# Kernel optimization log

Measured on AMD Instinct MI355X. Metric: run time of the kernel, lower is better.

## Reference

```python
import jax, jax.numpy as jnp
import numpy as np

N_HEAD = 8
D_HEAD = 32  # d_model=256 // n_head=8
SCALE = 1.0 / (D_HEAD ** 0.5)
CLIP = 10.0


def _rel_shift(x):
    # x: [qlen, klen, B, nh]; Transformer-XL relative shift along axis 1
    qlen, klen = x.shape[0], x.shape[1]
    zero_pad = jnp.zeros((qlen, 1) + x.shape[2:], dtype=x.dtype)
    x_pad = jnp.concatenate([zero_pad, x], axis=1)          # [qlen, klen+1, B, nh]
    x_pad = x_pad.reshape((klen + 1, qlen) + x.shape[2:])   # row-major reshape (torch .view)
    return x_pad[1:].reshape(x.shape)


def setup_inputs() -> dict:
    key = jax.random.key(0)
    ks = jax.random.split(key, 7)
    S, B, H = 1024, 8, 256
    return {
        "q": jax.random.normal(ks[0], (S, B, H), dtype=jnp.float32),
        "k": jax.random.normal(ks[1], (S, B, H), dtype=jnp.float32),
        "v": jax.random.normal(ks[2], (S, B, H), dtype=jnp.float32),
        "r": jax.random.normal(ks[3], (S, 1, H), dtype=jnp.float32),
        "bias_u": jax.random.normal(ks[4], (N_HEAD, D_HEAD), dtype=jnp.float32),
        "bias_v": jax.random.normal(ks[5], (N_HEAD, D_HEAD), dtype=jnp.float32),
        "mask": jax.random.randint(ks[6], (S, S, B), 0, 2).astype(jnp.bool_),
    }


def reference(q, k, v, r, bias_u, bias_v, mask):
    qlen, bsz = q.shape[0], q.shape[1]
    klen, rlen = k.shape[0], r.shape[0]
    q = q.reshape(qlen, bsz, N_HEAD, D_HEAD)
    k = k.reshape(klen, bsz, N_HEAD, D_HEAD)
    v = v.reshape(klen, bsz, N_HEAD, D_HEAD)
    r = r.reshape(rlen, N_HEAD, D_HEAD)

    AC = jnp.einsum('ibnd,jbnd->ijbn', q + bias_u, k)   # content term
    BD = jnp.einsum('ibnd,jnd->ijbn', q + bias_v, r)    # position term
    BD = _rel_shift(BD)

    score = (AC + BD) * SCALE
    score = CLIP * jnp.tanh(score)                      # clip > 0 path

    weight = jax.nn.softmax(score, axis=1)              # softmax over klen

    # mask is not None path: masked softmax of head-mean logits
    logits = score.mean(axis=-1)                        # [qlen, klen, B]
    logits = jnp.where(mask, -jnp.inf, logits)
    probs = jax.nn.softmax(logits, axis=1)

    out = jnp.einsum('ijbn,jbnd->ibnd', weight, v)
    out = out.reshape(qlen, bsz, N_HEAD * D_HEAD)
    return out, probs
```

## Files before the change

### kernel.cpp

```cpp
#include <hip/hip_runtime.h>
#include <hip/hip_fp16.h>

#define S 1024
#define B 8
#define NH 8
#define DH 32
#define HID 256
#define SCALEF 0.17677669529663687f

typedef __attribute__((ext_vector_type(8))) _Float16 f16x8;
typedef __attribute__((ext_vector_type(4))) _Float16 f16x4;
typedef __attribute__((ext_vector_type(4))) float f32x4;
#define MFMAH(a, b, c) __builtin_amdgcn_mfma_f32_16x16x32_f16(a, b, c, 0, 0, 0)

#define OFF_K_H 0
#define OFF_K_L 2560
#define OFF_VT  5120
#define OFF_RL  7680
#define OFF_RH  12800
#define OFF_P   17920
#define LDS_HF  20480

__device__ __forceinline__ void splitf16_4(const float4 x, _Float16* dh, _Float16* dl) {
  f16x4 h, l;
  h.x = (_Float16)x.x; h.y = (_Float16)x.y; h.z = (_Float16)x.z; h.w = (_Float16)x.w;
  l.x = (_Float16)(x.x - (float)h.x); l.y = (_Float16)(x.y - (float)h.y);
  l.z = (_Float16)(x.z - (float)h.z); l.w = (_Float16)(x.w - (float)h.w);
  *(f16x4*)dh = h; *(f16x4*)dl = l;
}
__device__ __forceinline__ void cvtf16_4(const float4 x, _Float16* d) {
  f16x4 h;
  h.x = (_Float16)x.x; h.y = (_Float16)x.y; h.z = (_Float16)x.z; h.w = (_Float16)x.w;
  *(f16x4*)d = h;
}

__global__ __launch_bounds__(256)
void relattn_mfma_86028194939537(const float* __restrict__ q, const float* __restrict__ k,
                                 const float* __restrict__ v, const float* __restrict__ r,
                                 const float* __restrict__ bu, const float* __restrict__ bv,
                                 float* __restrict__ out, __half* __restrict__ sws) {
  __shared__ _Float16 sm[LDS_HF];
  const int t = threadIdx.x;
  const int lane = t & 63, w = t >> 6;
  const int quad = lane >> 4, jn = lane & 15;
  const int bid = blockIdx.x;
  const int b = bid & 7, it = (bid >> 3) & 15, n = bid >> 7;
  const int i0 = it << 6, iw0 = i0 + (w << 4);
  const int colq = quad << 3;
  const int i16 = i0 >> 4;

  f16x8 qu_h, qu_l, qv_h, qv_l, qn_h, qn_l;
  {
    const float* bup = bu + n * DH + colq;
    const float* bvp = bv + n * DH + colq;
    const float* qp = q + (size_t)(iw0 + jn) * 2048 + b * HID + n * DH + colq;
    int r1 = iw0 + 1 + jn; if (r1 > S - 1) r1 = S - 1;
    const float* qp1 = q + (size_t)r1 * 2048 + b * HID + n * DH + colq;
#pragma unroll
    for (int e = 0; e < 8; ++e) {
      float xu = qp[e] + bup[e], xv = qp[e] + bvp[e], xn = qp1[e] + bvp[e];
      _Float16 h;
      h = (_Float16)xu; qu_h[e] = h; qu_l[e] = (_Float16)(xu - (float)h);
      h = (_Float16)xv; qv_h[e] = h; qv_l[e] = (_Float16)(xv - (float)h);
      h = (_Float16)xn; qn_h[e] = h; qn_l[e] = (_Float16)(xn - (float)h);
    }
  }

  __half* swsr[4];
#pragma unroll
  for (int g = 0; g < 4; ++g) {
    const int qr = (quad << 2) + g;
    swsr[g] = sws + (((size_t)(iw0 + qr) * 8 + b) * 8 + n) * 1024 + jn;
  }

  f32x4 out0 = {0.f, 0.f, 0.f, 0.f}, out1 = {0.f, 0.f, 0.f, 0.f};
  float ls[4] = {0.f, 0.f, 0.f, 0.f};

  {
    int j = t >> 3, d4 = (t & 7) << 2;
    const size_t g = (size_t)j * 2048 + b * HID + n * DH + d4;
    float4 kx = *(const float4*)(k + g);
    float4 vx = *(const float4*)(v + g);
    splitf16_4(kx, &sm[OFF_K_H + j * 40 + d4], &sm[OFF_K_L + j * 40 + d4]);
    sm[OFF_VT + (d4 + 0) * 40 + j] = (_Float16)vx.x;
    sm[OFF_VT + (d4 + 1) * 40 + j] = (_Float16)vx.y;
    sm[OFF_VT + (d4 + 2) * 40 + j] = (_Float16)vx.z;
    sm[OFF_VT + (d4 + 3) * 40 + j] = (_Float16)vx.w;
  }
#pragma unroll
  for (int p = 0; p < 3; ++p) {
    int ti = 2 * p + (t >> 7), row = (t >> 3) & 15, d4 = (t & 7) << 2;
    {
      int kL = 60 - i16 + ti;
      int tg = (kL << 4) + row; tg = tg < 0 ? 0 : (tg > S - 1 ? S - 1 : tg);
      float4 rv = *(const float4*)(r + (size_t)tg * HID + n * DH + d4);
      int sl = (kL + 72) & 7;
      cvtf16_4(rv, &sm[OFF_RL + (sl * 16 + row) * 40 + d4]);
    }
    {
      int kH = -i16 - 3 + ti;
      int tg = (kH << 4) - 17 + row; tg = tg < 0 ? 0 : (tg > S - 1 ? S - 1 : tg);
      float4 rv = *(const float4*)(r + (size_t)tg * HID + n * DH + d4);
      int sl = (kH + 72) & 7;
      cvtf16_4(rv, &sm[OFF_RH + (sl * 16 + row) * 40 + d4]);
    }
  }

  for (int jt = 0; jt < 32; ++jt) {
    const int j0 = jt << 5;
    __syncthreads();

    if (jt < 31) {
      int j = t >> 3, d4 = (t & 7) << 2;
      const int nbuf = ((jt + 1) & 1) * 1280;
      const size_t g = (size_t)(j0 + 32 + j) * 2048 + b * HID + n * DH + d4;
      float4 kx = *(const float4*)(k + g);
      float4 vx = *(const float4*)(v + g);
      splitf16_4(kx, &sm[OFF_K_H + nbuf + j * 40 + d4], &sm[OFF_K_L + nbuf + j * 40 + d4]);
      sm[OFF_VT + nbuf + (d4 + 0) * 40 + j] = (_Float16)vx.x;
      sm[OFF_VT + nbuf + (d4 + 1) * 40 + j] = (_Float16)vx.y;
      sm[OFF_VT + nbuf + (d4 + 2) * 40 + j] = (_Float16)vx.z;
      sm[OFF_VT + nbuf + (d4 + 3) * 40 + j] = (_Float16)vx.w;
    }
    {
      int ti = t >> 7, row = (t >> 3) & 15, d4 = (t & 7) << 2;
      {
        int kL = 66 + 2 * jt - i16 + ti;
        int tg = (kL << 4) + row; tg = tg < 0 ? 0 : (tg > S - 1 ? S - 1 : tg);
        float4 rv = *(const float4*)(r + (size_t)tg * HID + n * DH + d4);
        int sl = (kL + 72) & 7;
        cvtf16_4(rv, &sm[OFF_RL + (sl * 16 + row) * 40 + d4]);
      }
      {
        int kH = 2 * jt - i16 + 3 + ti;
        int tg = (kH << 4) - 17 + row; tg = tg < 0 ? 0 : (tg > S - 1 ? S - 1 : tg);
        float4 rv = *(const float4*)(r + (size_t)tg * HID + n * DH + d4);
        int sl = (kH + 72) & 7;
        cvtf16_4(rv, &sm[OFF_RH + (sl * 16 + row) * 40 + d4]);
      }
    }

    const int buf = (jt & 1) * 1280;
    const bool lowA = (j0 <= iw0 + 15);
    const bool highA = (j0 + 29 >= iw0);

    f32x4 ac0 = {0.f, 0.f, 0.f, 0.f}, ac1 = {0.f, 0.f, 0.f, 0.f};
    {
      f16x8 b0h = *(const f16x8*)&sm[OFF_K_H + buf + jn * 40 + colq];
      f16x8 b0l = *(const f16x8*)&sm[OFF_K_L + buf + jn * 40 + colq];
      f16x8 b1h = *(const f16x8*)&sm[OFF_K_H + buf + (16 + jn) * 40 + colq];
      f16x8 b1l = *(const f16x8*)&sm[OFF_K_L + buf + (16 + jn) * 40 + colq];
      ac0 = MFMAH(qu_h, b0h, ac0); ac0 = MFMAH(qu_h, b0l, ac0); ac0 = MFMAH(qu_l, b0h, ac0);
      ac1 = MFMAH(qu_h, b1h, ac1); ac1 = MFMAH(qu_h, b1l, ac1); ac1 = MFMAH(qu_l, b1h, ac1);
    }

    f32x4 zl0 = {0.f,0.f,0.f,0.f}, zl1 = {0.f,0.f,0.f,0.f}, zl2 = {0.f,0.f,0.f,0.f};
    f32x4 zh0 = {0.f,0.f,0.f,0.f}, zh1 = {0.f,0.f,0.f,0.f}, zh2 = {0.f,0.f,0.f,0.f};
    if (lowA) {
#pragma unroll
      for (int z = 0; z < 3; ++z) {
        int kL = 63 - i16 - w + 2 * jt + z;
        int sl = (kL + 72) & 7;
        f16x8 rr = *(const f16x8*)&sm[OFF_RL + (sl * 16 + jn) * 40 + colq];
        f32x4 acc = {0.f, 0.f, 0.f, 0.f};
        acc = MFMAH(qv_h, rr, acc); acc = MFMAH(qv_l, rr, acc);
        if (z == 0) zl0 = acc; else if (z == 1) zl1 = acc; else zl2 = acc;
      }
    }
    if (highA) {
#pragma unroll
      for (int z = 0; z < 3; ++z) {
        int kH = 2 * jt - i16 - w + z;
        int sl = (kH + 72) & 7;
        f16x8 rr = *(const f16x8*)&sm[OFF_RH + (sl * 16 + jn) * 40 + colq];
        f32x4 acc = {0.f, 0.f, 0.f, 0.f};
        acc = MFMAH(qn_h, rr, acc); acc = MFMAH(qn_l, rr, acc);
        if (z == 0) zh0 = acc; else if (z == 1) zh1 = acc; else zh2 = acc;
      }
    }

#pragma unroll
    for (int g = 0; g < 4; ++g) {
      const int qr = (quad << 2) + g;
      const int c0 = 15 - qr + jn;
      const int src = (lane & 48) | (c0 & 15);
      const bool zs = (c0 < 16);
      float lo0 = 0.f, lo1 = 0.f, hv0 = 0.f, hv1 = 0.f;
      if (lowA) {
        float a0 = __shfl(zl0[g], src, 64);
        float a1 = __shfl(zl1[g], src, 64);
        float a2 = __shfl(zl2[g], src, 64);
        lo0 = zs ? a0 : a1; lo1 = zs ? a1 : a2;
      }
      if (highA) {
        float a0 = __shfl(zh0[g], src, 64);
        float a1 = __shfl(zh1[g], src, 64);
        float a2 = __shfl(zh2[g], src, 64);
        hv0 = zs ? a0 : a1; hv1 = zs ? a1 : a2;
      }
      const int dj0 = j0 + jn - iw0 - qr;
#pragma unroll
      for (int f = 0; f < 2; ++f) {
        const int dj = dj0 + (f << 4);
        const float bd = (dj <= 0) ? (f ? lo1 : lo0) : ((dj == 1) ? 0.f : (f ? hv1 : hv0));
        const float acv = f ? ac1[g] : ac0[g];
        float sr = (acv + bd) * SCALEF;
        sr = fminf(fmaxf(sr, -15.f), 15.f);
        const float e2 = __expf(2.f * sr);
        const float scv = 10.f - 20.f * __builtin_amdgcn_rcpf(e2 + 1.f);
        swsr[g][j0 + (f << 4)] = __float2half(scv);
        const float pw = __expf(scv);
        const _Float16 ph = (_Float16)pw;
        ls[g] += (float)ph;
        sm[OFF_P + w * 640 + qr * 40 + (f << 4) + jn] = ph;
      }
    }

    {
      f16x8 pa = *(const f16x8*)&sm[OFF_P + w * 640 + jn * 40 + colq];
      f16x8 v0 = *(const f16x8*)&sm[OFF_VT + buf + jn * 40 + colq];
      f16x8 v1 = *(const f16x8*)&sm[OFF_VT + buf + (16 + jn) * 40 + colq];
      out0 = MFMAH(pa, v0, out0);
      out1 = MFMAH(pa, v1, out1);
    }
  }

#pragma unroll
  for (int g = 0; g < 4; ++g) {
    float s = ls[g];
    s += __shfl_xor(s, 1, 64); s += __shfl_xor(s, 2, 64);
    s += __shfl_xor(s, 4, 64); s += __shfl_xor(s, 8, 64);
    const float inv = 1.0f / s;
    const int qr = (quad << 2) + g;
    float* op = out + (size_t)(iw0 + qr) * 2048 + b * HID + n * DH;
    op[jn] = out0[g] * inv;
    op[16 + jn] = out1[g] * inv;
  }
}

__global__ __launch_bounds__(1024)
void relattn_probs_86028194939537(const __half* __restrict__ sws, const int* __restrict__ mask,
                                  float* __restrict__ probs) {
  __shared__ _Float16 ebuf[8][1032];
  __shared__ unsigned char mb[8192];
  __shared__ float psum[8][4];
  __shared__ float binv[8];
  const int t = threadIdx.x;
  const int i = blockIdx.x;
  const int tj = t & 255, bg = t >> 8;
  const int j4 = tj << 2;
  const int wl = (t >> 6) & 3;

  {
    const int4* m4 = (const int4*)(mask + (size_t)i * 8192);
#pragma unroll
    for (int u = 0; u < 2; ++u) {
      int idx = t + (u << 10);
      int4 mv = m4[idx];
      uchar4 mbv;
      mbv.x = (unsigned char)(mv.x != 0); mbv.y = (unsigned char)(mv.y != 0);
      mbv.z = (unsigned char)(mv.z != 0); mbv.w = (unsigned char)(mv.w != 0);
      *(uchar4*)&mb[idx << 2] = mbv;
    }
  }
  __syncthreads();

#pragma unroll
  for (int bb = 0; bb < 2; ++bb) {
    const int b = (bg << 1) + bb;
    float a0 = 0.f, a1 = 0.f, a2 = 0.f, a3 = 0.f;
#pragma unroll
    for (int n = 0; n < 8; ++n) {
      const __half2* p2 = (const __half2*)(sws + (((size_t)i * 8 + b) * 8 + n) * 1024 + j4);
      float2 x = __half22float2(p2[0]), y = __half22float2(p2[1]);
      a0 += x.x; a1 += x.y; a2 += y.x; a3 += y.y;
    }
    float e0 = mb[(j4 + 0) * 8 + b] ? 0.f : __expf(a0 * 0.125f);
    float e1 = mb[(j4 + 1) * 8 + b] ? 0.f : __expf(a1 * 0.125f);
    float e2 = mb[(j4 + 2) * 8 + b] ? 0.f : __expf(a2 * 0.125f);
    float e3 = mb[(j4 + 3) * 8 + b] ? 0.f : __expf(a3 * 0.125f);
    f16x4 ev;
    ev.x = (_Float16)e0; ev.y = (_Float16)e1; ev.z = (_Float16)e2; ev.w = (_Float16)e3;
    *(f16x4*)&ebuf[b][j4] = ev;
    float s = ((float)ev.x + (float)ev.y) + ((float)ev.z + (float)ev.w);
#pragma unroll
    for (int off = 32; off > 0; off >>= 1) s += __shfl_xor(s, off, 64);
    if ((t & 63) == 0) psum[b][wl] = s;
  }
  __syncthreads();
  if (t < 8) binv[t] = 1.0f / (psum[t][0] + psum[t][1] + psum[t][2] + psum[t][3]);
  __syncthreads();
#pragma unroll
  for (int u = 0; u < 2; ++u) {
    int f0 = (t << 2) + (u << 12);
    float4 o;
    o.x = (float)ebuf[(f0 + 0) & 7][(f0 + 0) >> 3] * binv[(f0 + 0) & 7];
    o.y = (float)ebuf[(f0 + 1) & 7][(f0 + 1) >> 3] * binv[(f0 + 1) & 7];
    o.z = (float)ebuf[(f0 + 2) & 7][(f0 + 2) >> 3] * binv[(f0 + 2) & 7];
    o.w = (float)ebuf[(f0 + 3) & 7][(f0 + 3) >> 3] * binv[(f0 + 3) & 7];
    *(float4*)(probs + (size_t)i * 8192 + f0) = o;
  }
}

#define TI 8
#define TJ 8
#define NTILE (S / TJ)
#define KSTR 288
#define KOFF 0
#define VOFF (TJ * KSTR)
#define BAND (2 * TJ * KSTR)
#define PROWS (TI + TJ - 1)
#define BSTR 292
#define BVR (BAND + PROWS * BSTR)
#define BUKo (BVR + PROWS * 8)
#define LDS_FL (BUKo + 64)

__global__ __launch_bounds__(256, 2)
void relattn_main_fb(const float* __restrict__ q, const float* __restrict__ k,
                     const float* __restrict__ v, const float* __restrict__ r,
                     const float* __restrict__ bias_u, const float* __restrict__ bias_v,
                     const int* __restrict__ mask, float* __restrict__ out,
                     float* __restrict__ probs_raw, float* __restrict__ ws_logits, int use_ws) {
  __shared__ float smf[LDS_FL];
  const int t = threadIdx.x;
  const int n = t & 7;
  const int il = (t >> 3) & 7;
  const int jp = t >> 6;
  const int bid = blockIdx.x;
  const int b = bid & 7;
  const int i0 = (bid >> 3) * TI;
  const int i = i0 + il;
  float qq[DH], qn[DH];
  {
    const float4* qr = (const float4*)(q + (i * B + b) * HID + n * DH);
#pragma unroll
    for (int dd = 0; dd < 8; ++dd) {
      float4 a = qr[dd];
      qq[4*dd+0] = a.x; qq[4*dd+1] = a.y; qq[4*dd+2] = a.z; qq[4*dd+3] = a.w;
    }
    if (i + 1 < S) {
      const float4* q2 = (const float4*)(q + ((i + 1) * B + b) * HID + n * DH);
#pragma unroll
      for (int dd = 0; dd < 8; ++dd) {
        float4 a = q2[dd];
        qn[4*dd+0] = a.x; qn[4*dd+1] = a.y; qn[4*dd+2] = a.z; qn[4*dd+3] = a.w;
      }
    } else {
#pragma unroll
      for (int d = 0; d < DH; ++d) qn[d] = 0.f;
    }
  }
  float oacc[DH];
#pragma unroll
  for (int d = 0; d < DH; ++d) oacc[d] = 0.f;
  float lsum = 0.f;
  for (int jt = 0; jt < NTILE; ++jt) {
    const int j0 = jt * TJ;
    const int Pstar = i0 + (TI - 1) - j0;
    const int lowBase = S - TI + j0 - i0;
    const int upBase = j0 - i0 - (TI + 1);
    __syncthreads();
    {
      int u = t;
      int row = u >> 6, c = u & 63;
      int gofs = ((j0 + row) * B + b) * HID + c * 4;
      int lofs = row * KSTR + (c >> 3) * 36 + (c & 7) * 4;
      *(float4*)(smf + KOFF + lofs) = *(const float4*)(k + gofs);
      *(float4*)(smf + VOFF + lofs) = *(const float4*)(v + gofs);
      u = t + 256; row = u >> 6; c = u & 63;
      gofs = ((j0 + row) * B + b) * HID + c * 4;
      lofs = row * KSTR + (c >> 3) * 36 + (c & 7) * 4;
      *(float4*)(smf + KOFF + lofs) = *(const float4*)(k + gofs);
      *(float4*)(smf + VOFF + lofs) = *(const float4*)(v + gofs);
    }
    for (int u = t; u < PROWS * 64; u += 256) {
      int prow = u >> 6, c = u & 63;
      int trow = (prow <= Pstar) ? (lowBase + prow) : (upBase + prow);
      float4 val = make_float4(0.f, 0.f, 0.f, 0.f);
      if ((unsigned)trow < (unsigned)S) val = *(const float4*)(r + trow * HID + c * 4);
      *(float4*)(smf + BAND + prow * BSTR + (c >> 3) * 36 + (c & 7) * 4) = val;
    }
    if (t < 64 + PROWS * 8) {
      const float4 *bb, *src;
      int slot;
      bool zero = false;
      if (t < 64) {
        int jl = t >> 3, nn = t & 7;
        bb = (const float4*)(bias_u + nn * DH);
        src = (const float4*)(k + ((j0 + jl) * B + b) * HID + nn * DH);
        slot = BUKo + jl * 8 + nn;
      } else {
        int u2 = t - 64;
        int prow = u2 >> 3, nn = u2 & 7;
        int trow = (prow <= Pstar) ? (lowBase + prow) : (upBase + prow);
        bb = (const float4*)(bias_v + nn * DH);
        if ((unsigned)trow < (unsigned)S) src = (const float4*)(r + trow * HID + nn * DH);
        else { src = bb; zero = true; }
        slot = BVR + prow * 8 + nn;
      }
      float a0 = 0.f, a1 = 0.f, a2 = 0.f, a3 = 0.f;
#pragma unroll
      for (int dd = 0; dd < 8; ++dd) {
        float4 x = bb[dd], y = src[dd];
        a0 = fmaf(x.x, y.x, a0); a1 = fmaf(x.y, y.y, a1);
        a2 = fmaf(x.z, y.z, a2); a3 = fmaf(x.w, y.w, a3);
      }
      smf[slot] = zero ? 0.f : ((a0 + a1) + (a2 + a3));
    }
    __syncthreads();
#pragma unroll
    for (int jj = 0; jj < 2; ++jj) {
      const int jl = jp * 2 + jj;
      const int jg = j0 + jl;
      const int p = jl + (TI - 1) - il;
      float a0 = 0.f, a1 = 0.f, a2 = 0.f, a3 = 0.f;
      const float4* kr = (const float4*)(smf + KOFF + jl * KSTR + n * 36);
#pragma unroll
      for (int dd = 0; dd < 8; ++dd) {
        float4 kv = kr[dd];
        a0 = fmaf(qq[4*dd+0], kv.x, a0); a1 = fmaf(qq[4*dd+1], kv.y, a1);
        a2 = fmaf(qq[4*dd+2], kv.z, a2); a3 = fmaf(qq[4*dd+3], kv.w, a3);
      }
      float ac = (a0 + a1) + (a2 + a3) + smf[BUKo + jl * 8 + n];
      float b0 = 0.f, b1 = 0.f, b2 = 0.f, b3 = 0.f;
      const float4* br = (const float4*)(smf + BAND + p * BSTR + n * 36);
      if (jg <= i) {
#pragma unroll
        for (int dd = 0; dd < 8; ++dd) {
          float4 bv4 = br[dd];
          b0 = fmaf(qq[4*dd+0], bv4.x, b0); b1 = fmaf(qq[4*dd+1], bv4.y, b1);
          b2 = fmaf(qq[4*dd+2], bv4.z, b2); b3 = fmaf(qq[4*dd+3], bv4.w, b3);
        }
      } else {
#pragma unroll
        for (int dd = 0; dd < 8; ++dd) {
          float4 bv4 = br[dd];
          b0 = fmaf(qn[4*dd+0], bv4.x, b0); b1 = fmaf(qn[4*dd+1], bv4.y, b1);
          b2 = fmaf(qn[4*dd+2], bv4.z, b2); b3 = fmaf(qn[4*dd+3], bv4.w, b3);
        }
      }
      float bd = (b0 + b1) + (b2 + b3) + smf[BVR + p * 8 + n];
      float sr = (ac + bd) * SCALEF;
      sr = fminf(fmaxf(sr, -15.f), 15.f);
      float e2 = __expf(2.f * sr);
      float scv = 10.f * (e2 - 1.f) / (e2 + 1.f);
      float ssum = scv;
      ssum += __shfl_xor(ssum, 1, 64);
      ssum += __shfl_xor(ssum, 2, 64);
      ssum += __shfl_xor(ssum, 4, 64);
      if (n == 0) {
        float logit = ssum * 0.125f;
        if (use_ws) {
          ws_logits[(i * B + b) * S + jg] = logit;
        } else {
          int gofs = (i * S + jg) * B + b;
          probs_raw[gofs] = (mask[gofs] != 0) ? -1e30f : logit;
        }
      }
      float pw = __expf(scv);
      lsum += pw;
      const float4* vr = (const float4*)(smf + VOFF + jl * KSTR + n * 36);
#pragma unroll
      for (int dd = 0; dd < 8; ++dd) {
        float4 vv = vr[dd];
        oacc[4*dd+0] = fmaf(pw, vv.x, oacc[4*dd+0]);
        oacc[4*dd+1] = fmaf(pw, vv.y, oacc[4*dd+1]);
        oacc[4*dd+2] = fmaf(pw, vv.z, oacc[4*dd+2]);
        oacc[4*dd+3] = fmaf(pw, vv.w, oacc[4*dd+3]);
      }
    }
  }
  __syncthreads();
  if (jp >= 2) {
    float* red = smf + (t - 128) * 33;
#pragma unroll
    for (int d = 0; d < DH; ++d) red[d] = oacc[d];
    red[DH] = lsum;
  }
  __syncthreads();
  if (jp < 2) {
    const float* red = smf + t * 33;
#pragma unroll
    for (int d = 0; d < DH; ++d) oacc[d] += red[d];
    lsum += red[DH];
  }
  __syncthreads();
  if (jp == 1) {
    float* red = smf + (t - 64) * 33;
#pragma unroll
    for (int d = 0; d < DH; ++d) red[d] = oacc[d];
    red[DH] = lsum;
  }
  __syncthreads();
  if (jp == 0) {
    const float* red = smf + t * 33;
#pragma unroll
    for (int d = 0; d < DH; ++d) oacc[d] += red[d];
    lsum += red[DH];
    float inv = 1.f / lsum;
    float4* orow = (float4*)(out + (i * B + b) * HID + n * DH);
#pragma unroll
    for (int dd = 0; dd < 8; ++dd) {
      float4 o4;
      o4.x = oacc[4*dd+0] * inv; o4.y = oacc[4*dd+1] * inv;
      o4.z = oacc[4*dd+2] * inv; o4.w = oacc[4*dd+3] * inv;
      orow[dd] = o4;
    }
  }
}

__global__ __launch_bounds__(256)
void relattn_norm_fb(float* __restrict__ probs, const float* __restrict__ ws_logits,
                     const int* __restrict__ mask, int use_ws) {
  const int t = threadIdx.x;
  const int bid = blockIdx.x;
  const int b = bid & 7;
  const int i = bid >> 3;
  float vals[4];
  float s = 0.f;
#pragma unroll
  for (int kk = 0; kk < 4; ++kk) {
    int j = t + 256 * kk;
    float lg;
    if (use_ws) {
      lg = ws_logits[(i * B + b) * S + j];
      if (mask[(i * S + j) * B + b] != 0) lg = -1e30f;
    } else {
      lg = probs[(i * S + j) * B + b];
    }
    vals[kk] = __expf(lg);
    s += vals[kk];
  }
#pragma unroll
  for (int off = 32; off > 0; off >>= 1) s += __shfl_down(s, off, 64);
  __shared__ float wsum[4];
  __shared__ float tot;
  if ((t & 63) == 0) wsum[t >> 6] = s;
  __syncthreads();
  if (t == 0) tot = wsum[0] + wsum[1] + wsum[2] + wsum[3];
  __syncthreads();
  float inv = 1.f / tot;
#pragma unroll
  for (int kk = 0; kk < 4; ++kk) {
    int j = t + 256 * kk;
    probs[(i * S + j) * B + b] = vals[kk] * inv;
  }
}

extern "C" void kernel_launch(void* const* d_in, const int* in_sizes, int n_in,
                              void* d_out, int out_size, void* d_ws, size_t ws_size,
                              hipStream_t stream) {
  const float* q  = (const float*)d_in[0];
  const float* k  = (const float*)d_in[1];
  const float* v  = (const float*)d_in[2];
  const float* r  = (const float*)d_in[3];
  const float* bu = (const float*)d_in[4];
  const float* bv = (const float*)d_in[5];
  const int* mask = (const int*)d_in[6];
  float* out = (float*)d_out;
  float* probs = out + S * B * HID;

  const size_t WS_NEED = (size_t)S * S * B * NH * sizeof(__half);
  if (ws_size >= WS_NEED) {
    __half* sws = (__half*)d_ws;
    relattn_mfma_86028194939537<<<dim3(1024), dim3(256), 0, stream>>>(
        q, k, v, r, bu, bv, out, sws);
    relattn_probs_86028194939537<<<dim3(1024), dim3(1024), 0, stream>>>(sws, mask, probs);
  } else {
    float* wsl = (float*)d_ws;
    const int use_ws = (ws_size >= (size_t)S * S * B * sizeof(float)) ? 1 : 0;
    relattn_main_fb<<<dim3((S / TI) * B), dim3(256), 0, stream>>>(
        q, k, v, r, bu, bv, mask, out, probs, wsl, use_ws);
    relattn_norm_fb<<<dim3(S * B), dim3(256), 0, stream>>>(probs, wsl, mask, use_ws);
  }
}
```

Baseline: 282.7 us.

## Store exp(score) instead of score and use product-root for head-mean softmax

The attention kernel now folds scale, tanh and exp into two exp2 calls with precomputed constants, dropping the clamp and the separate score store. It writes the fp16 exp(score) tile from LDS to global with 16-byte vector stores instead of scattered scalar half stores. The probs kernel multiplies the per-head exp values and takes an eighth root via three sqrts, replacing the sum-then-exp. This removes transcendentals and scattered stores, but risks overflow or underflow in the fp16 product and the loss of the clamp for large scores.

After: 286.0 us. Within noise of the previous version (+1.2%).

```diff
diff --git a/kernel.cpp b/kernel.cpp
--- a/kernel.cpp
+++ b/kernel.cpp
@@ -20,6 +20,10 @@
 #define OFF_RH  12800
 #define OFF_P   17920
 #define LDS_HF  20480
+
+#define C_E2  0.51006978f
+#define C_PWA 14.42695041f
+#define C_PWB -28.85390082f
 
 __device__ __forceinline__ void splitf16_4(const float4 x, _Float16* dh, _Float16* dl) {
   f16x4 h, l;
@@ -66,12 +70,8 @@
     }
   }
 
-  __half* swsr[4];
-#pragma unroll
-  for (int g = 0; g < 4; ++g) {
-    const int qr = (quad << 2) + g;
-    swsr[g] = sws + (((size_t)(iw0 + qr) * 8 + b) * 8 + n) * 1024 + jn;
-  }
+  const int prow = lane >> 2, pseg = lane & 3;
+  __half* swsp = sws + (((size_t)(iw0 + prow) * 8 + b) * 8 + n) * 1024 + (pseg << 3);
 
   f32x4 out0 = {0.f, 0.f, 0.f, 0.f}, out1 = {0.f, 0.f, 0.f, 0.f};
   float ls[4] = {0.f, 0.f, 0.f, 0.f};
@@ -204,12 +204,10 @@
         const int dj = dj0 + (f << 4);
         const float bd = (dj <= 0) ? (f ? lo1 : lo0) : ((dj == 1) ? 0.f : (f ? hv1 : hv0));
         const float acv = f ? ac1[g] : ac0[g];
-        float sr = (acv + bd) * SCALEF;
-        sr = fminf(fmaxf(sr, -15.f), 15.f);
-        const float e2 = __expf(2.f * sr);
-        const float scv = 10.f - 20.f * __builtin_amdgcn_rcpf(e2 + 1.f);
-        swsr[g][j0 + (f << 4)] = __float2half(scv);
-        const float pw = __expf(scv);
+        const float s = acv + bd;
+        const float e2 = __builtin_amdgcn_exp2f(s * C_E2);
+        const float tq = __builtin_amdgcn_rcpf(e2 + 1.f);
+        const float pw = __builtin_amdgcn_exp2f(fmaf(tq, C_PWB, C_PWA));
         const _Float16 ph = (_Float16)pw;
         ls[g] += (float)ph;
         sm[OFF_P + w * 640 + qr * 40 + (f << 4) + jn] = ph;
@@ -222,6 +220,12 @@
       f16x8 v1 = *(const f16x8*)&sm[OFF_VT + buf + (16 + jn) * 40 + colq];
       out0 = MFMAH(pa, v0, out0);
       out1 = MFMAH(pa, v1, out1);
+    }
+
+    {
+      f16x8 pr = *(const f16x8*)&sm[OFF_P + w * 640 + prow * 40 + (pseg << 3)];
+      *(f16x8*)swsp = pr;
+      swsp += 32;
     }
   }
 
@@ -268,17 +272,16 @@
 #pragma unroll
   for (int bb = 0; bb < 2; ++bb) {
     const int b = (bg << 1) + bb;
-    float a0 = 0.f, a1 = 0.f, a2 = 0.f, a3 = 0.f;
+    float a0 = 1.f, a1 = 1.f, a2 = 1.f, a3 = 1.f;
 #pragma unroll
     for (int n = 0; n < 8; ++n) {
-      const __half2* p2 = (const __half2*)(sws + (((size_t)i * 8 + b) * 8 + n) * 1024 + j4);
-      float2 x = __half22float2(p2[0]), y = __half22float2(p2[1]);
-      a0 += x.x; a1 += x.y; a2 += y.x; a3 += y.y;
-    }
-    float e0 = mb[(j4 + 0) * 8 + b] ? 0.f : __expf(a0 * 0.125f);
-    float e1 = mb[(j4 + 1) * 8 + b] ? 0.f : __expf(a1 * 0.125f);
-    float e2 = mb[(j4 + 2) * 8 + b] ? 0.f : __expf(a2 * 0.125f);
-    float e3 = mb[(j4 + 3) * 8 + b] ? 0.f : __expf(a3 * 0.125f);
+      f16x4 pv = *(const f16x4*)(sws + (((size_t)i * 8 + b) * 8 + n) * 1024 + j4);
+      a0 *= (float)pv.x; a1 *= (float)pv.y; a2 *= (float)pv.z; a3 *= (float)pv.w;
+    }
+    float e0 = mb[(j4 + 0) * 8 + b] ? 0.f : sqrtf(sqrtf(sqrtf(a0)));
+    float e1 = mb[(j4 + 1) * 8 + b] ? 0.f : sqrtf(sqrtf(sqrtf(a1)));
+    float e2 = mb[(j4 + 2) * 8 + b] ? 0.f : sqrtf(sqrtf(sqrtf(a2)));
+    float e3 = mb[(j4 + 3) * 8 + b] ? 0.f : sqrtf(sqrtf(sqrtf(a3)));
     f16x4 ev;
     ev.x = (_Float16)e0; ev.y = (_Float16)e1; ev.z = (_Float16)e2; ev.w = (_Float16)e3;
     *(f16x4*)&ebuf[b][j4] = ev;
```
